# Optimization experiments

Measured on AMD Instinct MI355X. Metric: run time of the kernel, lower is better.

The kernel has to match this reference:

```python
import jax, jax.numpy as jnp
import numpy as np

BN_EPS = 1e-5

def _per_sample_conv(x, w, stride):
    # x: [B,C,H,W], w: [B,O,I,kh,kw] -> per-sample conv2d, padding=1
    def one(xi, wi):
        return jax.lax.conv_general_dilated(
            xi[None], wi, window_strides=(stride, stride),
            padding=[(1, 1), (1, 1)],
            dimension_numbers=('NCHW', 'OIHW', 'NCHW'))[0]
    return jax.vmap(one)(x, w)

def _batchnorm(x, gamma, beta):
    # training-mode BN over (B,H,W) per channel
    mean = x.mean(axis=(0, 2, 3), keepdims=True)
    var = x.var(axis=(0, 2, 3), keepdims=True)
    xhat = (x - mean) * jax.lax.rsqrt(var + BN_EPS)
    return xhat * gamma[None, :, None, None] + beta[None, :, None, None]

def setup_inputs() -> dict:
    key = jax.random.key(0)
    k1, k2, k3 = jax.random.split(key, 3)
    B, C, H, W, K = 64, 128, 56, 56, 3
    x = jax.random.normal(k1, (B, C, H, W), dtype=jnp.float32)
    conv1_w = jax.random.normal(k2, (B, C, C, K, K), dtype=jnp.float32) * 0.05
    conv2_w = jax.random.normal(k3, (B, C, C, K, K), dtype=jnp.float32) * 0.05
    return {
        'x': x, 'conv1_w': conv1_w, 'conv2_w': conv2_w,
        'gamma1': jnp.ones((C,), jnp.float32), 'beta1': jnp.zeros((C,), jnp.float32),
        'gamma2': jnp.ones((C,), jnp.float32), 'beta2': jnp.zeros((C,), jnp.float32),
    }

def reference(x, conv1_w, conv2_w, gamma1, beta1, gamma2, beta2):
    residual = x  # downsample=False -> identity residual, stride 1
    out = _per_sample_conv(x, conv1_w, stride=1)
    out = jax.nn.relu(_batchnorm(out, gamma1, beta1))
    out = _per_sample_conv(out, conv2_w, stride=1)
    out = _batchnorm(out, gamma2, beta2)
    out = jax.nn.relu(out + residual)
    return out
```

## Files before the change

kernel.cpp:

```cpp
#include <hip/hip_runtime.h>
#include <hip/hip_bf16.h>
#include <stdint.h>
#include <stddef.h>

#define CH 128
#define HH 56
#define WW 56
#define HWPIX (HH*WW)
#define NB 64
#define NPIXF 200704.0f
#define NCONVBLK 896
#define PSTR 72

typedef __attribute__((ext_vector_type(8))) short short8v;
typedef __attribute__((ext_vector_type(8))) unsigned short bfv8;
typedef __attribute__((ext_vector_type(4))) unsigned short bfv4;
typedef __attribute__((ext_vector_type(4))) float f32x4;

__device__ __forceinline__ unsigned short f2bf(float f) {
  unsigned int u = __float_as_uint(f);
  u += 0x7fffu + ((u >> 16) & 1u);
  return (unsigned short)(u >> 16);
}
__device__ __forceinline__ float bf2f(unsigned short s) {
  return __uint_as_float(((unsigned int)s) << 16);
}

__global__ __launch_bounds__(256)
void prep_x(const float* __restrict__ x, unsigned short* __restrict__ xT) {
  __shared__ unsigned short tile[4 * 56 * 128];
  const int bid = blockIdx.x;
  const int b = bid / 14, hq = bid % 14;
  const int hl = threadIdx.x >> 6;
  const int h = hq * 4 + hl;
  const int w = threadIdx.x & 63;
  if (w < WW) {
    const float* src = x + (size_t)b * CH * HWPIX + h * WW + w;
    const int pos = hl * WW + w;
    #pragma unroll 4
    for (int c0 = 0; c0 < CH; c0 += 8) {
      bfv8 v;
      #pragma unroll
      for (int k = 0; k < 8; ++k) v[k] = f2bf(src[(size_t)(c0 + k) * HWPIX]);
      const int idx = (pos * CH + c0) ^ ((pos & 7) << 3);
      *(bfv8*)(tile + idx) = v;
    }
  }
  __syncthreads();
  unsigned short* out = xT + (size_t)(b * HH + hq * 4) * WW * CH;
  #pragma unroll
  for (int j = 0; j < 14; ++j) {
    const int u = j * 256 + threadIdx.x;
    const int idx = (u * 8) ^ (((u >> 4) & 7) << 3);
    *(bfv8*)(out + u * 8) = *(const bfv8*)(tile + idx);
  }
}

__global__ __launch_bounds__(256)
void prep_w(const float* __restrict__ w1, const float* __restrict__ w2,
            unsigned short* __restrict__ o1, unsigned short* __restrict__ o2) {
  __shared__ unsigned short lw[18432];
  const int id = blockIdx.x;
  const int which = id >> 9;
  const int b = (id >> 3) & 63, ck = id & 7;
  const float* src = (which ? w2 : w1) + ((size_t)b * 16384 + ck * 2048) * 9;
  unsigned short* dst = (which ? o2 : o1);
  const int t = threadIdx.x;
  #pragma unroll
  for (int j = 0; j < 72; ++j)
    lw[j * 256 + t] = f2bf(src[j * 256 + t]);
  __syncthreads();
  const int ol = t >> 4, oct = t & 15;
  #pragma unroll
  for (int tap = 0; tap < 9; ++tap) {
    bfv8 v;
    #pragma unroll
    for (int k = 0; k < 8; ++k) v[k] = lw[(ol * 128 + oct * 8 + k) * 9 + tap];
    *(bfv8*)(dst + ((size_t)(b * 9 + tap) * CH + ck * 16 + ol) * CH + oct * 8) = v;
  }
}

template<bool FUSE>
__global__ __launch_bounds__(256, 2)
void conv_kernel(const unsigned short* __restrict__ in,
                 const unsigned short* __restrict__ wt,
                 unsigned short* __restrict__ outp,
                 float* __restrict__ partials,
                 const float* __restrict__ tab) {
  __shared__ __align__(16) unsigned short patch[300 * PSTR];
  __shared__ __align__(16) unsigned short wbuf[12288];
  __shared__ float sacc[256];
  const int xcd = blockIdx.x & 7;
  const int q = blockIdx.x >> 3;
  const int s = q / 14;
  const int tile = q - s * 14;
  const int b = s * 8 + xcd;
  const int ty = tile / 7, tx = tile % 7;
  const int h0 = ty * 28, w0 = tx * 8;
  const int t = threadIdx.x;

  const int lane = t & 63, wv = t >> 6;
  const int lrow = lane & 15, lgrp = lane >> 4;
  const int px = lrow & 7, pyl = lrow >> 3;

  sacc[t] = 0.0f;

  const unsigned short* wsrc =
      wt + (size_t)b * 9 * CH * CH + (wv * 32 + lrow) * CH + lgrp * 8;

#define STAGE(S, P) { \
    const unsigned short* g_ = wsrc + (((S) % 18) >> 1) * (CH * CH) + \
                               ((S) / 18) * 64 + ((S) & 1) * 32; \
    unsigned short* l_ = wbuf + (wv * 3 + (P)) * 1024; \
    __builtin_amdgcn_global_load_lds( \
        (const __attribute__((address_space(1))) void*)g_, \
        (__attribute__((address_space(3))) void*)l_, 16, 0, 0); \
    __builtin_amdgcn_global_load_lds( \
        (const __attribute__((address_space(1))) void*)(g_ + 16 * CH), \
        (__attribute__((address_space(3))) void*)(l_ + 512), 16, 0, 0); \
  }

#define STAGE_PATCH(PH) { \
    for (int u = t; u < 300; u += 256) { \
      const int dh = u / 10, dw = u - dh * 10; \
      const int h = h0 + dh - 1, w = w0 + dw - 1; \
      unsigned short* ld = &patch[u * PSTR]; \
      if (h >= 0 && h < HH && w >= 0 && w < WW) { \
        const unsigned short* src = \
            in + ((size_t)((b * HH + h) * WW + w)) * CH + (PH) * 64; \
        if (FUSE) { \
          for (int j = 0; j < 8; ++j) { \
            const bfv8 v = *(const bfv8*)(src + j * 8); \
            bfv8 o; \
            for (int k = 0; k < 8; ++k) { \
              const int c = (PH) * 64 + j * 8 + k; \
              o[k] = f2bf(fmaxf(bf2f(v[k]) * tab[c] + tab[CH + c], 0.0f)); \
            } \
            *(bfv8*)(ld + j * 8) = o; \
          } \
        } else { \
          for (int j = 0; j < 8; ++j) \
            *(bfv8*)(ld + j * 8) = *(const bfv8*)(src + j * 8); \
        } \
      } else { \
        const bfv8 z = {0, 0, 0, 0, 0, 0, 0, 0}; \
        for (int j = 0; j < 8; ++j) *(bfv8*)(ld + j * 8) = z; \
      } \
    } }

#define COMPUTE(S, P) { \
    const int tap_ = ((S) % 18) >> 1, icl_ = (S) & 1; \
    const int pb_ = (pyl + tap_ / 3) * 10 + px + tap_ % 3; \
    const unsigned short* ab_ = wbuf + (wv * 3 + (P)) * 1024 + lane * 8; \
    const short8v a0_ = *(const short8v*)(ab_); \
    const short8v a1_ = *(const short8v*)(ab_ + 512); \
    _Pragma("unroll") \
    for (int nf = 0; nf < 14; ++nf) { \
      const short8v bfr = *(const short8v*)( \
          &patch[(pb_ + nf * 20) * PSTR + icl_ * 32 + lgrp * 8]); \
      acc[0][nf] = __builtin_amdgcn_mfma_f32_16x16x32_bf16(a0_, bfr, acc[0][nf], 0, 0, 0); \
      acc[1][nf] = __builtin_amdgcn_mfma_f32_16x16x32_bf16(a1_, bfr, acc[1][nf], 0, 0, 0); \
    } }

#define RUN(S) \
    __builtin_amdgcn_sched_barrier(0); \
    STAGE((S) + 2, ((S) + 2) % 3) \
    asm volatile("s_waitcnt vmcnt(4)" ::: "memory"); \
    __builtin_amdgcn_sched_barrier(0); \
    COMPUTE(S, (S) % 3)

  STAGE(0, 0)
  STAGE_PATCH(0)
  __syncthreads();

  f32x4 acc[2][14];
  #pragma unroll
  for (int m = 0; m < 2; ++m)
    #pragma unroll
    for (int n = 0; n < 14; ++n) acc[m][n] = (f32x4){0.f, 0.f, 0.f, 0.f};

  STAGE(1, 1)
  RUN(0)  RUN(1)  RUN(2)  RUN(3)  RUN(4)  RUN(5)  RUN(6)  RUN(7)
  RUN(8)  RUN(9)  RUN(10) RUN(11) RUN(12) RUN(13) RUN(14) RUN(15)
  __builtin_amdgcn_sched_barrier(0);
  asm volatile("s_waitcnt vmcnt(2)" ::: "memory");
  __builtin_amdgcn_sched_barrier(0);
  COMPUTE(16, 1)
  __builtin_amdgcn_sched_barrier(0);
  asm volatile("s_waitcnt vmcnt(0)" ::: "memory");
  __builtin_amdgcn_sched_barrier(0);
  COMPUTE(17, 2)

  STAGE(18, 0)
  __syncthreads();
  STAGE_PATCH(1)
  __syncthreads();

  STAGE(19, 1)
  RUN(18) RUN(19) RUN(20) RUN(21) RUN(22) RUN(23) RUN(24) RUN(25)
  RUN(26) RUN(27) RUN(28) RUN(29) RUN(30) RUN(31) RUN(32) RUN(33)
  __builtin_amdgcn_sched_barrier(0);
  asm volatile("s_waitcnt vmcnt(2)" ::: "memory");
  __builtin_amdgcn_sched_barrier(0);
  COMPUTE(34, 1)
  __builtin_amdgcn_sched_barrier(0);
  asm volatile("s_waitcnt vmcnt(0)" ::: "memory");
  __builtin_amdgcn_sched_barrier(0);
  COMPUTE(35, 2)
#undef RUN
#undef COMPUTE
#undef STAGE
#undef STAGE_PATCH

  __syncthreads();

  #pragma unroll
  for (int mf = 0; mf < 2; ++mf) {
    f32x4 sv4 = {0.f, 0.f, 0.f, 0.f}, qv4 = {0.f, 0.f, 0.f, 0.f};
    #pragma unroll
    for (int nf = 0; nf < 14; ++nf) {
      const f32x4 v = acc[mf][nf];
      sv4 += v;
      qv4 += v * v;
    }
    #pragma unroll
    for (int r = 0; r < 4; ++r) {
      float sv = sv4[r], qv = qv4[r];
      sv += __shfl_xor(sv, 1, 64);  qv += __shfl_xor(qv, 1, 64);
      sv += __shfl_xor(sv, 2, 64);  qv += __shfl_xor(qv, 2, 64);
      sv += __shfl_xor(sv, 4, 64);  qv += __shfl_xor(qv, 4, 64);
      sv += __shfl_xor(sv, 8, 64);  qv += __shfl_xor(qv, 8, 64);
      if (lrow == 0) {
        const int ch = wv * 32 + mf * 16 + lgrp * 4 + r;
        atomicAdd(&sacc[ch], sv);
        atomicAdd(&sacc[CH + ch], qv);
      }
    }
  }

  char* obuf = (char*)patch;
  #pragma unroll
  for (int a = 0; a < 2; ++a) {
    if (a) __syncthreads();
    #pragma unroll
    for (int mf = 0; mf < 2; ++mf) {
      #pragma unroll
      for (int m = 0; m < 7; ++m) {
        const f32x4 v = acc[mf][a * 7 + m];
        bfv4 pk;
        #pragma unroll
        for (int r = 0; r < 4; ++r) pk[r] = f2bf(v[r]);
        const int p = (m * 2 + pyl) * 8 + px;
        const int ch = wv * 32 + mf * 16 + lgrp * 4;
        int byte = p * 256 + ch * 2;
        byte ^= ((byte >> 8) & 3) << 5;
        *(bfv4*)(obuf + byte) = pk;
      }
    }
    __syncthreads();
    if (a == 0) partials[(size_t)blockIdx.x * 256 + t] = sacc[t];
    #pragma unroll
    for (int j = 0; j < 7; ++j) {
      const int u = j * 256 + t;
      int byte = u * 16;
      byte ^= ((byte >> 8) & 3) << 5;
      const bfv8 v = *(const bfv8*)(obuf + byte);
      const int pix = u >> 4, py = pix >> 3, pxx = pix & 7;
      *(bfv8*)(outp + ((size_t)((b * HH + h0 + a * 14 + py) * WW + (w0 + pxx))) * CH +
               (u & 15) * 8) = v;
    }
  }
}

__global__ __launch_bounds__(256)
void stat_reduce(const float* __restrict__ partials, float* __restrict__ st) {
  const int t = threadIdx.x;
  float s = 0.0f;
  const int i0 = blockIdx.x * (NCONVBLK / 32);
  for (int i = 0; i < NCONVBLK / 32; ++i)
    s += partials[(size_t)(i0 + i) * 256 + t];
  atomicAdd(&st[t], s);
}

__global__ __launch_bounds__(128)
void bn_stats(const float* __restrict__ st, const float* __restrict__ gamma,
              const float* __restrict__ beta, float* __restrict__ tab) {
  const int c = threadIdx.x;
  const float inv = 1.0f / NPIXF;
  const float mean = st[c] * inv;
  const float var = st[CH + c] * inv - mean * mean;
  const float s = gamma[c] / sqrtf(var + 1e-5f);
  tab[c] = s;
  tab[CH + c] = beta[c] - mean * s;
}

template<bool BF16RES>
__global__ __launch_bounds__(256)
void final_kernel(const unsigned short* __restrict__ y2,
                  const unsigned short* __restrict__ xbf,
                  const float* __restrict__ x,
                  const float* __restrict__ tab, float* __restrict__ out) {
  __shared__ float tile[CH * 113];
  const int bid = blockIdx.x;
  const int b = bid / 28, hp = bid % 28;
  const int h0 = hp * 2;
  const int t = threadIdx.x;

  if (t < 224) {
    const int pix = t >> 1, half = t & 1;
    const int h = h0 + pix / 56, w = pix % 56;
    const size_t base = ((size_t)((b * HH + h) * WW + w)) * CH + half * 64;
    const unsigned short* ys = y2 + base;
    const unsigned short* rs = xbf + base;
    const float* xs = x + (size_t)b * CH * HWPIX + h * WW + w;
    #pragma unroll
    for (int j = 0; j < 8; ++j) {
      const bfv8 v = *(const bfv8*)(ys + j * 8);
      bfv8 r;
      if (BF16RES) r = *(const bfv8*)(rs + j * 8);
      #pragma unroll
      for (int k = 0; k < 8; ++k) {
        const int c = half * 64 + j * 8 + k;
        const float res = BF16RES ? bf2f(r[k]) : xs[(size_t)c * HWPIX];
        tile[c * 113 + pix] =
            fmaxf(bf2f(v[k]) * tab[c] + tab[CH + c] + res, 0.0f);
      }
    }
  }
  __syncthreads();

  const int w = t & 63, hl = (t >> 6) & 1, cg = t >> 7;
  if (w < WW) {
    const int pos = hl * 56 + w;
    float* os = out + (size_t)b * CH * HWPIX + (size_t)(h0 + hl) * WW + w;
    #pragma unroll
    for (int c0 = 0; c0 < 64; ++c0) {
      const int c = cg * 64 + c0;
      os[(size_t)c * HWPIX] = tile[c * 113 + pos];
    }
  }
}

extern "C" void kernel_launch(void* const* d_in, const int* in_sizes, int n_in,
                              void* d_out, int out_size, void* d_ws, size_t ws_size,
                              hipStream_t stream) {
  const float* x  = (const float*)d_in[0];
  const float* w1 = (const float*)d_in[1];
  const float* w2 = (const float*)d_in[2];
  const float* g1 = (const float*)d_in[3];
  const float* b1 = (const float*)d_in[4];
  const float* g2 = (const float*)d_in[5];
  const float* b2 = (const float*)d_in[6];
  float* out = (float*)d_out;

  char* ws = (char*)d_ws;
  unsigned short* xT  = (unsigned short*)(ws);
  unsigned short* y1  = (unsigned short*)(ws + 51380224);
  unsigned short* w1b = (unsigned short*)(ws + 102760448);
  unsigned short* w2b = (unsigned short*)(ws + 121634816);
  float*          p1  = (float*)(ws + 140509184);
  float*          p2  = (float*)(ws + 143720448);
  float*          st  = (float*)(ws + 146931712);
  const bool sepY2 = ws_size >= (size_t)146935808 + 51380224;
  unsigned short* y2  = sepY2 ? (unsigned short*)(ws + 146935808) : xT;

  (void)hipMemsetAsync(st, 0, 2048, stream);

  hipLaunchKernelGGL(prep_x, dim3(NB * 14), dim3(256), 0, stream, x, xT);
  hipLaunchKernelGGL(prep_w, dim3(1024), dim3(256), 0, stream, w1, w2, w1b, w2b);
  hipLaunchKernelGGL((conv_kernel<false>), dim3(NCONVBLK), dim3(256), 0, stream,
                     xT, w1b, y1, p1, (const float*)nullptr);
  hipLaunchKernelGGL(stat_reduce, dim3(32), dim3(256), 0, stream, p1, st);
  hipLaunchKernelGGL(bn_stats, dim3(1), dim3(128), 0, stream, st, g1, b1, st + 512);
  hipLaunchKernelGGL((conv_kernel<true>), dim3(NCONVBLK), dim3(256), 0, stream,
                     y1, w2b, y2, p2, st + 512);
  hipLaunchKernelGGL(stat_reduce, dim3(32), dim3(256), 0, stream, p2, st + 256);
  hipLaunchKernelGGL(bn_stats, dim3(1), dim3(128), 0, stream, st + 256, g2, b2, st + 768);
  if (sepY2) {
    hipLaunchKernelGGL((final_kernel<true>), dim3(NB * 28), dim3(256), 0, stream,
                       y2, xT, x, st + 768, out);
  } else {
    hipLaunchKernelGGL((final_kernel<false>), dim3(NB * 28), dim3(256), 0, stream,
                       y2, xT, x, st + 768, out);
  }
}
```

Before: 273.9 us.

## Enlarge conv tile to full-height column with 512-thread blocks

Each conv block now covers a full 56-row by 8-column strip using 8 waves, with 448 blocks instead of 896. Each wave owns 16 output channels and 28 pixel fragments, so every weight fragment is reused across twice as many MFMAs. This cuts vertical halo duplication and the weight staging per wave. In exchange, each patch fragment read from LDS now feeds one MFMA instead of two, doubling LDS reads for the B operand. The larger patch also raises LDS use per block, which may lower how many blocks fit on a CU.

```diff
diff --git a/kernel.cpp b/kernel.cpp
--- a/kernel.cpp
+++ b/kernel.cpp
@@ -9,7 +9,7 @@
 #define HWPIX (HH*WW)
 #define NB 64
 #define NPIXF 200704.0f
-#define NCONVBLK 896
+#define NCONVBLK 448
 #define PSTR 72
 
 typedef __attribute__((ext_vector_type(8))) short short8v;
@@ -81,49 +81,45 @@
 }
 
 template<bool FUSE>
-__global__ __launch_bounds__(256, 2)
+__global__ __launch_bounds__(512, 2)
 void conv_kernel(const unsigned short* __restrict__ in,
                  const unsigned short* __restrict__ wt,
                  unsigned short* __restrict__ outp,
                  float* __restrict__ partials,
                  const float* __restrict__ tab) {
-  __shared__ __align__(16) unsigned short patch[300 * PSTR];
+  __shared__ __align__(16) unsigned short patch[580 * PSTR];
   __shared__ __align__(16) unsigned short wbuf[12288];
   __shared__ float sacc[256];
   const int xcd = blockIdx.x & 7;
   const int q = blockIdx.x >> 3;
-  const int s = q / 14;
-  const int tile = q - s * 14;
+  const int s = q / 7;
+  const int col = q - s * 7;
   const int b = s * 8 + xcd;
-  const int ty = tile / 7, tx = tile % 7;
-  const int h0 = ty * 28, w0 = tx * 8;
+  const int w0 = col * 8;
   const int t = threadIdx.x;
 
   const int lane = t & 63, wv = t >> 6;
   const int lrow = lane & 15, lgrp = lane >> 4;
   const int px = lrow & 7, pyl = lrow >> 3;
 
-  sacc[t] = 0.0f;
+  if (t < 256) sacc[t] = 0.0f;
 
   const unsigned short* wsrc =
-      wt + (size_t)b * 9 * CH * CH + (wv * 32 + lrow) * CH + lgrp * 8;
+      wt + (size_t)b * 9 * CH * CH + (wv * 16 + lrow) * CH + lgrp * 8;
 
 #define STAGE(S, P) { \
     const unsigned short* g_ = wsrc + (((S) % 18) >> 1) * (CH * CH) + \
                                ((S) / 18) * 64 + ((S) & 1) * 32; \
-    unsigned short* l_ = wbuf + (wv * 3 + (P)) * 1024; \
+    unsigned short* l_ = wbuf + (wv * 3 + (P)) * 512; \
     __builtin_amdgcn_global_load_lds( \
         (const __attribute__((address_space(1))) void*)g_, \
         (__attribute__((address_space(3))) void*)l_, 16, 0, 0); \
-    __builtin_amdgcn_global_load_lds( \
-        (const __attribute__((address_space(1))) void*)(g_ + 16 * CH), \
-        (__attribute__((address_space(3))) void*)(l_ + 512), 16, 0, 0); \
   }
 
 #define STAGE_PATCH(PH) { \
-    for (int u = t; u < 300; u += 256) { \
+    for (int u = t; u < 580; u += 512) { \
       const int dh = u / 10, dw = u - dh * 10; \
-      const int h = h0 + dh - 1, w = w0 + dw - 1; \
+      const int h = dh - 1, w = w0 + dw - 1; \
       unsigned short* ld = &patch[u * PSTR]; \
       if (h >= 0 && h < HH && w >= 0 && w < WW) { \
         const unsigned short* src = \
@@ -151,21 +147,19 @@
 #define COMPUTE(S, P) { \
     const int tap_ = ((S) % 18) >> 1, icl_ = (S) & 1; \
     const int pb_ = (pyl + tap_ / 3) * 10 + px + tap_ % 3; \
-    const unsigned short* ab_ = wbuf + (wv * 3 + (P)) * 1024 + lane * 8; \
+    const unsigned short* ab_ = wbuf + (wv * 3 + (P)) * 512 + lane * 8; \
     const short8v a0_ = *(const short8v*)(ab_); \
-    const short8v a1_ = *(const short8v*)(ab_ + 512); \
     _Pragma("unroll") \
-    for (int nf = 0; nf < 14; ++nf) { \
+    for (int nf = 0; nf < 28; ++nf) { \
       const short8v bfr = *(const short8v*)( \
           &patch[(pb_ + nf * 20) * PSTR + icl_ * 32 + lgrp * 8]); \
-      acc[0][nf] = __builtin_amdgcn_mfma_f32_16x16x32_bf16(a0_, bfr, acc[0][nf], 0, 0, 0); \
-      acc[1][nf] = __builtin_amdgcn_mfma_f32_16x16x32_bf16(a1_, bfr, acc[1][nf], 0, 0, 0); \
+      acc[nf] = __builtin_amdgcn_mfma_f32_16x16x32_bf16(a0_, bfr, acc[nf], 0, 0, 0); \
     } }
 
 #define RUN(S) \
     __builtin_amdgcn_sched_barrier(0); \
     STAGE((S) + 2, ((S) + 2) % 3) \
-    asm volatile("s_waitcnt vmcnt(4)" ::: "memory"); \
+    asm volatile("s_waitcnt vmcnt(2)" ::: "memory"); \
     __builtin_amdgcn_sched_barrier(0); \
     COMPUTE(S, (S) % 3)
 
@@ -173,17 +167,15 @@
   STAGE_PATCH(0)
   __syncthreads();
 
-  f32x4 acc[2][14];
-  #pragma unroll
-  for (int m = 0; m < 2; ++m)
-    #pragma unroll
-    for (int n = 0; n < 14; ++n) acc[m][n] = (f32x4){0.f, 0.f, 0.f, 0.f};
+  f32x4 acc[28];
+  #pragma unroll
+  for (int n = 0; n < 28; ++n) acc[n] = (f32x4){0.f, 0.f, 0.f, 0.f};
 
   STAGE(1, 1)
   RUN(0)  RUN(1)  RUN(2)  RUN(3)  RUN(4)  RUN(5)  RUN(6)  RUN(7)
   RUN(8)  RUN(9)  RUN(10) RUN(11) RUN(12) RUN(13) RUN(14) RUN(15)
   __builtin_amdgcn_sched_barrier(0);
-  asm volatile("s_waitcnt vmcnt(2)" ::: "memory");
+  asm volatile("s_waitcnt vmcnt(1)" ::: "memory");
   __builtin_amdgcn_sched_barrier(0);
   COMPUTE(16, 1)
   __builtin_amdgcn_sched_barrier(0);
@@ -200,7 +192,7 @@
   RUN(18) RUN(19) RUN(20) RUN(21) RUN(22) RUN(23) RUN(24) RUN(25)
   RUN(26) RUN(27) RUN(28) RUN(29) RUN(30) RUN(31) RUN(32) RUN(33)
   __builtin_amdgcn_sched_barrier(0);
-  asm volatile("s_waitcnt vmcnt(2)" ::: "memory");
+  asm volatile("s_waitcnt vmcnt(1)" ::: "memory");
   __builtin_amdgcn_sched_barrier(0);
   COMPUTE(34, 1)
   __builtin_amdgcn_sched_barrier(0);
@@ -214,12 +206,11 @@
 
   __syncthreads();
 
-  #pragma unroll
-  for (int mf = 0; mf < 2; ++mf) {
+  {
     f32x4 sv4 = {0.f, 0.f, 0.f, 0.f}, qv4 = {0.f, 0.f, 0.f, 0.f};
     #pragma unroll
-    for (int nf = 0; nf < 14; ++nf) {
-      const f32x4 v = acc[mf][nf];
+    for (int nf = 0; nf < 28; ++nf) {
+      const f32x4 v = acc[nf];
       sv4 += v;
       qv4 += v * v;
     }
@@ -231,9 +222,9 @@
       sv += __shfl_xor(sv, 4, 64);  qv += __shfl_xor(qv, 4, 64);
       sv += __shfl_xor(sv, 8, 64);  qv += __shfl_xor(qv, 8, 64);
       if (lrow == 0) {
-        const int ch = wv * 32 + mf * 16 + lgrp * 4 + r;
-        atomicAdd(&sacc[ch], sv);
-        atomicAdd(&sacc[CH + ch], qv);
+        const int ch = wv * 16 + lgrp * 4 + r;
+        sacc[ch] = sv;
+        sacc[CH + ch] = qv;
       }
     }
   }
@@ -243,30 +234,27 @@
   for (int a = 0; a < 2; ++a) {
     if (a) __syncthreads();
     #pragma unroll
-    for (int mf = 0; mf < 2; ++mf) {
+    for (int m = 0; m < 14; ++m) {
+      const f32x4 v = acc[a * 14 + m];
+      bfv4 pk;
       #pragma unroll
-      for (int m = 0; m < 7; ++m) {
-        const f32x4 v = acc[mf][a * 7 + m];
-        bfv4 pk;
-        #pragma unroll
-        for (int r = 0; r < 4; ++r) pk[r] = f2bf(v[r]);
-        const int p = (m * 2 + pyl) * 8 + px;
-        const int ch = wv * 32 + mf * 16 + lgrp * 4;
-        int byte = p * 256 + ch * 2;
-        byte ^= ((byte >> 8) & 3) << 5;
-        *(bfv4*)(obuf + byte) = pk;
-      }
+      for (int r = 0; r < 4; ++r) pk[r] = f2bf(v[r]);
+      const int p = (m * 2 + pyl) * 8 + px;
+      const int ch = wv * 16 + lgrp * 4;
+      int byte = p * 256 + ch * 2;
+      byte ^= ((byte >> 8) & 3) << 5;
+      *(bfv4*)(obuf + byte) = pk;
     }
     __syncthreads();
-    if (a == 0) partials[(size_t)blockIdx.x * 256 + t] = sacc[t];
+    if (a == 0 && t < 256) partials[(size_t)blockIdx.x * 256 + t] = sacc[t];
     #pragma unroll
     for (int j = 0; j < 7; ++j) {
-      const int u = j * 256 + t;
+      const int u = j * 512 + t;
       int byte = u * 16;
       byte ^= ((byte >> 8) & 3) << 5;
       const bfv8 v = *(const bfv8*)(obuf + byte);
       const int pix = u >> 4, py = pix >> 3, pxx = pix & 7;
-      *(bfv8*)(outp + ((size_t)((b * HH + h0 + a * 14 + py) * WW + (w0 + pxx))) * CH +
+      *(bfv8*)(outp + ((size_t)((b * HH + a * 28 + py) * WW + (w0 + pxx))) * CH +
                (u & 15) * 8) = v;
     }
   }
@@ -368,11 +356,11 @@
 
   hipLaunchKernelGGL(prep_x, dim3(NB * 14), dim3(256), 0, stream, x, xT);
   hipLaunchKernelGGL(prep_w, dim3(1024), dim3(256), 0, stream, w1, w2, w1b, w2b);
-  hipLaunchKernelGGL((conv_kernel<false>), dim3(NCONVBLK), dim3(256), 0, stream,
+  hipLaunchKernelGGL((conv_kernel<false>), dim3(NCONVBLK), dim3(512), 0, stream,
                      xT, w1b, y1, p1, (const float*)nullptr);
   hipLaunchKernelGGL(stat_reduce, dim3(32), dim3(256), 0, stream, p1, st);
   hipLaunchKernelGGL(bn_stats, dim3(1), dim3(128), 0, stream, st, g1, b1, st + 512);
-  hipLaunchKernelGGL((conv_kernel<true>), dim3(NCONVBLK), dim3(256), 0, stream,
+  hipLaunchKernelGGL((conv_kernel<true>), dim3(NCONVBLK), dim3(512), 0, stream,
                      y1, w2b, y2, p2, st + 512);
   hipLaunchKernelGGL(stat_reduce, dim3(32), dim3(256), 0, stream, p2, st + 256);
   hipLaunchKernelGGL(bn_stats, dim3(1), dim3(128), 0, stream, st + 256, g2, b2, st + 768);
```

After: 352.4 us. +28.6%, slower.
